# Performance work log

Measured on AMD Instinct MI355X. Metric: run time of the kernel, lower is better.

The kernel has to match this reference:

```python
import jax, jax.numpy as jnp
import numpy as np

B, S, DIM = 4, 4096, 1024
H, HD = 16, 64  # n_heads, head_dim = dim // n_heads
UMV = 20.0      # unified_max_value (init kwarg)


def setup_inputs() -> dict:
    key = jax.random.key(0)
    kx, kw = jax.random.split(key)
    x = jax.random.normal(kx, (B, S, DIM), dtype=jnp.float32)
    # qkv_proj: Linear(dim, 3*dim). Small weight scale + positive bias keeps
    # attention scores inside the keep-window [0, 2*UMV] so denominators are safe.
    W_qkv = jax.random.normal(kw, (DIM, 3 * DIM), dtype=jnp.float32) * 0.02
    b_qkv = jnp.full((3 * DIM,), 0.5, dtype=jnp.float32)
    return {"x": x, "W_qkv": W_qkv, "b_qkv": b_qkv}


def reference(x, W_qkv, b_qkv):
    Bb, Ss, _ = x.shape
    qkv = x @ W_qkv + b_qkv                      # [B,S,3*dim]
    qkv = qkv.reshape(Bb, Ss, H, 3 * HD)          # [B,S,H,3*hd]
    Q, K, V = jnp.split(qkv, 3, axis=-1)          # each [B,S,H,hd]
    # matmul(Q, K.transpose(-2,-1)) on [B,S,H,hd]: contract head_dim -> [B,S,H,H]
    s = jnp.einsum('bshd,bsgd->bshg', Q, K) - UMV
    e = jnp.exp(s)
    mask = (s > UMV) | (s < -UMV)                 # keep only s in [-UMV, UMV]
    e = jnp.where(mask, 0.0, e)
    denom = jnp.sum(e, axis=-1, keepdims=True)
    p = e / denom                                  # [B,S,H,H]
    out = jnp.einsum('bshg,bsgd->bshd', p, V)      # [B,S,H,hd]
    return out
```

## Files before the change

kernel.cpp:

```cpp
#include <hip/hip_runtime.h>

typedef _Float16 v8h __attribute__((ext_vector_type(8)));
typedef _Float16 v4h __attribute__((ext_vector_type(4)));
typedef _Float16 v2h __attribute__((ext_vector_type(2)));
typedef float v4f __attribute__((ext_vector_type(4)));

__device__ __forceinline__ void gl16(const void* g, void* l) {
    __builtin_amdgcn_global_load_lds(
        (const __attribute__((address_space(1))) unsigned int*)g,
        (__attribute__((address_space(3))) unsigned int*)l, 16, 0, 0);
}

__global__ __launch_bounds__(256) void k_cvt_x(const float* __restrict__ x,
                                               _Float16* __restrict__ x16) {
    int i = (blockIdx.x * 256 + threadIdx.x) * 8;
    float4 a = *(const float4*)(x + i);
    float4 b = *(const float4*)(x + i + 4);
    v8h h;
    h[0] = (_Float16)a.x; h[1] = (_Float16)a.y; h[2] = (_Float16)a.z; h[3] = (_Float16)a.w;
    h[4] = (_Float16)b.x; h[5] = (_Float16)b.y; h[6] = (_Float16)b.z; h[7] = (_Float16)b.w;
    *(v8h*)(x16 + i) = h;
}

__global__ __launch_bounds__(256) void k_cvt_w(const float* __restrict__ W,
                                               _Float16* __restrict__ Wt) {
    __shared__ float T[64][68];
    int k0 = (blockIdx.x & 15) * 64;
    int n0 = (blockIdx.x >> 4) * 64;
    int t = threadIdx.x;
    int tr = t >> 4;
    int tc = t & 15;
#pragma unroll
    for (int rr = 0; rr < 4; rr++) {
        int kk = rr * 16 + tr;
        float4 v = *(const float4*)(W + (size_t)(k0 + kk) * 3072 + n0 + tc * 4);
        T[kk][tc * 4 + 0] = v.x; T[kk][tc * 4 + 1] = v.y;
        T[kk][tc * 4 + 2] = v.z; T[kk][tc * 4 + 3] = v.w;
    }
    __syncthreads();
#pragma unroll
    for (int ww = 0; ww < 4; ww++) {
        int nn = ww * 16 + tr;
        v4h h;
#pragma unroll
        for (int i = 0; i < 4; i++) h[i] = (_Float16)T[tc * 4 + i][nn];
        *(v4h*)(Wt + (size_t)(n0 + nn) * 1024 + k0 + tc * 4) = h;
    }
}

__global__ __launch_bounds__(256) void k_gemm(const _Float16* __restrict__ A,
                                              const _Float16* __restrict__ Bt,
                                              const float* __restrict__ bias,
                                              _Float16* __restrict__ C) {
    __shared__ __align__(16) _Float16 As[128 * 32];
    __shared__ __align__(16) _Float16 Bs[128 * 32];
    int bm = blockIdx.x & 127;
    int bn = blockIdx.x >> 7;
    int m0 = bm * 128, n0 = bn * 128;
    int tid = threadIdx.x;
    int w = tid >> 6, lane = tid & 63;
    int quad = lane >> 4, l15 = lane & 15;
    int wm = (w & 1) * 64, wn = (w >> 1) * 64;

    int mc1 = w * 16 + (lane >> 2);
    int mc2 = (w + 4) * 16 + (lane >> 2);
    int k8 = (lane & 3) * 8;
    const _Float16* aS1 = A + (size_t)(m0 + mc1) * 1024 + k8;
    const _Float16* aS2 = A + (size_t)(m0 + mc2) * 1024 + k8;
    const _Float16* bS1 = Bt + (size_t)(n0 + mc1) * 1024 + k8;
    const _Float16* bS2 = Bt + (size_t)(n0 + mc2) * 1024 + k8;
    _Float16* lA1 = &As[w * 512];
    _Float16* lA2 = &As[(w + 4) * 512];
    _Float16* lB1 = &Bs[w * 512];
    _Float16* lB2 = &Bs[(w + 4) * 512];

    v4f acc[4][4] = {};

    for (int kt = 0; kt < 1024; kt += 32) {
        __syncthreads();
        gl16(aS1 + kt, lA1);
        gl16(aS2 + kt, lA2);
        gl16(bS1 + kt, lB1);
        gl16(bS2 + kt, lB2);
        __syncthreads();
        v8h af[4], bf[4];
#pragma unroll
        for (int mi = 0; mi < 4; mi++)
            af[mi] = *(const v8h*)&As[(wm + mi * 16 + l15) * 32 + quad * 8];
#pragma unroll
        for (int ni = 0; ni < 4; ni++)
            bf[ni] = *(const v8h*)&Bs[(wn + ni * 16 + l15) * 32 + quad * 8];
#pragma unroll
        for (int mi = 0; mi < 4; mi++)
#pragma unroll
            for (int ni = 0; ni < 4; ni++)
                acc[mi][ni] = __builtin_amdgcn_mfma_f32_16x16x32_f16(af[mi], bf[ni], acc[mi][ni], 0, 0, 0);
    }

#pragma unroll
    for (int ni = 0; ni < 4; ni++) {
        int n = n0 + wn + ni * 16 + l15;
        float bv = bias[n];
#pragma unroll
        for (int mi = 0; mi < 4; mi++) {
            int mbase = m0 + wm + mi * 16 + quad * 4;
#pragma unroll
            for (int r = 0; r < 4; r++)
                C[(size_t)(mbase + r) * 3072 + n] = (_Float16)(acc[mi][ni][r] + bv);
        }
    }
}

__global__ __launch_bounds__(256) void k_attn(const _Float16* __restrict__ qkv,
                                              float* __restrict__ out) {
    __shared__ __align__(16) _Float16 Lh[4][16 * 200];
    __shared__ float Pb[4][16 * 17];
    int tid = threadIdx.x;
    int w = tid >> 6, lane = tid & 63;
    int pos = blockIdx.x * 4 + w;
    _Float16* L = Lh[w];
    float* P = Pb[w];
    const _Float16* src = qkv + (size_t)pos * 3072;

#pragma unroll
    for (int ii = 0; ii < 6; ii++) {
        int e = (ii * 64 + lane) * 8;
        v8h v = *(const v8h*)(src + e);
        int h = e / 192, r = e % 192;
        *(v8h*)(L + h * 200 + r) = v;
    }
    __syncthreads();

    {
        int h = lane & 15, quad = lane >> 4;
        const _Float16* Qr = L + h * 200;
        v8h q[8];
#pragma unroll
        for (int d = 0; d < 8; d++) q[d] = *(const v8h*)(Qr + d * 8);
        float e4[4];
#pragma unroll
        for (int c = 0; c < 4; c++) {
            const _Float16* Kr = L + (quad * 4 + c) * 200 + 64;
            float a = 0.f;
#pragma unroll
            for (int d = 0; d < 8; d++) {
                v8h k = *(const v8h*)(Kr + d * 8);
#pragma unroll
                for (int j = 0; j < 4; j++)
                    a = __builtin_amdgcn_fdot2(((v2h*)&q[d])[j], ((v2h*)&k)[j], a, false);
            }
            float s = a - 20.0f;
            e4[c] = (s > 20.0f || s < -20.0f) ? 0.0f : __expf(s);
        }
        float part = e4[0] + e4[1] + e4[2] + e4[3];
        part += __shfl_xor(part, 16, 64);
        part += __shfl_xor(part, 32, 64);
        float inv = 1.0f / part;
#pragma unroll
        for (int c = 0; c < 4; c++) P[h * 17 + quad * 4 + c] = e4[c] * inv;
    }
    __syncthreads();

    {
        int h2 = lane >> 2, db = (lane & 3) * 16;
        float o[16];
#pragma unroll
        for (int i = 0; i < 16; i++) o[i] = 0.f;
#pragma unroll
        for (int g = 0; g < 16; g++) {
            float p = P[h2 * 17 + g];
            const _Float16* Vr = L + g * 200 + 128 + db;
            v8h v0 = *(const v8h*)(Vr);
            v8h v1 = *(const v8h*)(Vr + 8);
#pragma unroll
            for (int i = 0; i < 8; i++) {
                o[i]     += p * (float)v0[i];
                o[8 + i] += p * (float)v1[i];
            }
        }
        float* dst = out + (size_t)pos * 1024 + h2 * 64 + db;
#pragma unroll
        for (int d4 = 0; d4 < 4; d4++) {
            float4 v;
            v.x = o[d4 * 4 + 0]; v.y = o[d4 * 4 + 1];
            v.z = o[d4 * 4 + 2]; v.w = o[d4 * 4 + 3];
            *(float4*)(dst + d4 * 4) = v;
        }
    }
}

extern "C" void kernel_launch(void* const* d_in, const int* in_sizes, int n_in,
                              void* d_out, int out_size, void* d_ws, size_t ws_size,
                              hipStream_t stream) {
    (void)in_sizes; (void)n_in; (void)out_size; (void)ws_size;
    const float* x  = (const float*)d_in[0];
    const float* Wq = (const float*)d_in[1];
    const float* bq = (const float*)d_in[2];
    float* out = (float*)d_out;

    char* ws = (char*)d_ws;
    _Float16* x16   = (_Float16*)ws;
    _Float16* wt16  = (_Float16*)(ws + (32u << 20));
    _Float16* qkv16 = (_Float16*)(ws + (38u << 20));

    k_cvt_x<<<8192, 256, 0, stream>>>(x, x16);
    k_cvt_w<<<768, 256, 0, stream>>>(Wq, wt16);
    k_gemm<<<3072, 256, 0, stream>>>(x16, wt16, bq, qkv16);
    k_attn<<<4096, 256, 0, stream>>>(qkv16, out);
}
```

Before: 283.8 us.

## Fuse x fp16 conversion into GEMM, use wave-local fences and fp16 PV accumulation

Removes the separate x-to-fp16 kernel: the GEMM now loads fp32 x directly, converts it in registers and stores it to LDS, which avoids a full write and re-read of a 32 MB intermediate. In the attention kernel, the block-wide __syncthreads calls become per-wave lgkmcnt waits, since each wave only touches its own LDS slice. The P·V accumulation moves to packed fp16 FMA instead of fp32, which halves the arithmetic but costs output precision. The GEMM's A-tile loads change from async global-to-LDS to synchronous register loads, which may expose more load latency, and each A tile is now re-read as fp32 by every n-block (24 times).

```diff
diff --git a/kernel.cpp b/kernel.cpp
--- a/kernel.cpp
+++ b/kernel.cpp
@@ -11,15 +11,8 @@
         (__attribute__((address_space(3))) unsigned int*)l, 16, 0, 0);
 }
 
-__global__ __launch_bounds__(256) void k_cvt_x(const float* __restrict__ x,
-                                               _Float16* __restrict__ x16) {
-    int i = (blockIdx.x * 256 + threadIdx.x) * 8;
-    float4 a = *(const float4*)(x + i);
-    float4 b = *(const float4*)(x + i + 4);
-    v8h h;
-    h[0] = (_Float16)a.x; h[1] = (_Float16)a.y; h[2] = (_Float16)a.z; h[3] = (_Float16)a.w;
-    h[4] = (_Float16)b.x; h[5] = (_Float16)b.y; h[6] = (_Float16)b.z; h[7] = (_Float16)b.w;
-    *(v8h*)(x16 + i) = h;
+__device__ __forceinline__ void wave_lds_fence() {
+    asm volatile("s_waitcnt lgkmcnt(0)" ::: "memory");
 }
 
 __global__ __launch_bounds__(256) void k_cvt_w(const float* __restrict__ W,
@@ -48,7 +41,7 @@
     }
 }
 
-__global__ __launch_bounds__(256) void k_gemm(const _Float16* __restrict__ A,
+__global__ __launch_bounds__(256) void k_gemm(const float* __restrict__ x,
                                               const _Float16* __restrict__ Bt,
                                               const float* __restrict__ bias,
                                               _Float16* __restrict__ C) {
@@ -62,15 +55,17 @@
     int quad = lane >> 4, l15 = lane & 15;
     int wm = (w & 1) * 64, wn = (w >> 1) * 64;
 
+    int idx1 = tid, idx2 = tid + 256;
+    const float* aF1 = x + (size_t)(m0 + (idx1 >> 2)) * 1024 + (idx1 & 3) * 8;
+    const float* aF2 = x + (size_t)(m0 + (idx2 >> 2)) * 1024 + (idx2 & 3) * 8;
+    _Float16* lA1 = &As[idx1 * 8];
+    _Float16* lA2 = &As[idx2 * 8];
+
     int mc1 = w * 16 + (lane >> 2);
     int mc2 = (w + 4) * 16 + (lane >> 2);
     int k8 = (lane & 3) * 8;
-    const _Float16* aS1 = A + (size_t)(m0 + mc1) * 1024 + k8;
-    const _Float16* aS2 = A + (size_t)(m0 + mc2) * 1024 + k8;
     const _Float16* bS1 = Bt + (size_t)(n0 + mc1) * 1024 + k8;
     const _Float16* bS2 = Bt + (size_t)(n0 + mc2) * 1024 + k8;
-    _Float16* lA1 = &As[w * 512];
-    _Float16* lA2 = &As[(w + 4) * 512];
     _Float16* lB1 = &Bs[w * 512];
     _Float16* lB2 = &Bs[(w + 4) * 512];
 
@@ -78,10 +73,19 @@
 
     for (int kt = 0; kt < 1024; kt += 32) {
         __syncthreads();
-        gl16(aS1 + kt, lA1);
-        gl16(aS2 + kt, lA2);
+        float4 f0 = *(const float4*)(aF1 + kt);
+        float4 f1 = *(const float4*)(aF1 + kt + 4);
+        float4 f2 = *(const float4*)(aF2 + kt);
+        float4 f3 = *(const float4*)(aF2 + kt + 4);
         gl16(bS1 + kt, lB1);
         gl16(bS2 + kt, lB2);
+        v8h h0, h1;
+        h0[0] = (_Float16)f0.x; h0[1] = (_Float16)f0.y; h0[2] = (_Float16)f0.z; h0[3] = (_Float16)f0.w;
+        h0[4] = (_Float16)f1.x; h0[5] = (_Float16)f1.y; h0[6] = (_Float16)f1.z; h0[7] = (_Float16)f1.w;
+        h1[0] = (_Float16)f2.x; h1[1] = (_Float16)f2.y; h1[2] = (_Float16)f2.z; h1[3] = (_Float16)f2.w;
+        h1[4] = (_Float16)f3.x; h1[5] = (_Float16)f3.y; h1[6] = (_Float16)f3.z; h1[7] = (_Float16)f3.w;
+        *(v8h*)lA1 = h0;
+        *(v8h*)lA2 = h1;
         __syncthreads();
         v8h af[4], bf[4];
 #pragma unroll
@@ -129,7 +133,7 @@
         int h = e / 192, r = e % 192;
         *(v8h*)(L + h * 200 + r) = v;
     }
-    __syncthreads();
+    wave_lds_fence();
 
     {
         int h = lane & 15, quad = lane >> 4;
@@ -159,31 +163,32 @@
 #pragma unroll
         for (int c = 0; c < 4; c++) P[h * 17 + quad * 4 + c] = e4[c] * inv;
     }
-    __syncthreads();
+    wave_lds_fence();
 
     {
         int h2 = lane >> 2, db = (lane & 3) * 16;
-        float o[16];
-#pragma unroll
-        for (int i = 0; i < 16; i++) o[i] = 0.f;
+        v2h o2[8] = {};
 #pragma unroll
         for (int g = 0; g < 16; g++) {
-            float p = P[h2 * 17 + g];
+            _Float16 ph = (_Float16)P[h2 * 17 + g];
+            v2h p2; p2[0] = ph; p2[1] = ph;
             const _Float16* Vr = L + g * 200 + 128 + db;
             v8h v0 = *(const v8h*)(Vr);
             v8h v1 = *(const v8h*)(Vr + 8);
 #pragma unroll
-            for (int i = 0; i < 8; i++) {
-                o[i]     += p * (float)v0[i];
-                o[8 + i] += p * (float)v1[i];
+            for (int j = 0; j < 4; j++) {
+                o2[j]     = p2 * ((v2h*)&v0)[j] + o2[j];
+                o2[4 + j] = p2 * ((v2h*)&v1)[j] + o2[4 + j];
             }
         }
         float* dst = out + (size_t)pos * 1024 + h2 * 64 + db;
 #pragma unroll
         for (int d4 = 0; d4 < 4; d4++) {
             float4 v;
-            v.x = o[d4 * 4 + 0]; v.y = o[d4 * 4 + 1];
-            v.z = o[d4 * 4 + 2]; v.w = o[d4 * 4 + 3];
+            v.x = (float)o2[d4 * 2][0];
+            v.y = (float)o2[d4 * 2][1];
+            v.z = (float)o2[d4 * 2 + 1][0];
+            v.w = (float)o2[d4 * 2 + 1][1];
             *(float4*)(dst + d4 * 4) = v;
         }
     }
@@ -199,12 +204,10 @@
     float* out = (float*)d_out;
 
     char* ws = (char*)d_ws;
-    _Float16* x16   = (_Float16*)ws;
-    _Float16* wt16  = (_Float16*)(ws + (32u << 20));
-    _Float16* qkv16 = (_Float16*)(ws + (38u << 20));
-
-    k_cvt_x<<<8192, 256, 0, stream>>>(x, x16);
+    _Float16* wt16  = (_Float16*)ws;
+    _Float16* qkv16 = (_Float16*)(ws + (8u << 20));
+
     k_cvt_w<<<768, 256, 0, stream>>>(Wq, wt16);
-    k_gemm<<<3072, 256, 0, stream>>>(x16, wt16, bq, qkv16);
+    k_gemm<<<3072, 256, 0, stream>>>(x, wt16, bq, qkv16);
     k_attn<<<4096, 256, 0, stream>>>(qkv16, out);
 }
```

Result: slower. 315.3 us (+11.1%).
